# Optimization experiments

Measured on AMD Instinct MI355X. Metric: run time of the kernel, lower is better.

The kernel has to match this reference:

```python
import jax, jax.numpy as jnp
import numpy as np

ALPHA = 1.702
LIMIT = 7.0
EPS = 1e-5
TOP_K = 4


def setup_inputs() -> dict:
    key = jax.random.key(0)
    ks = jax.random.split(key, 8)
    B, S, H, I, E = 2, 512, 2048, 2048, 16
    return {
        "x": jax.random.normal(ks[0], (B, S, H), jnp.float32),
        "norm_w": jnp.ones((H,), jnp.float32),
        "gate_w": jax.random.normal(ks[1], (E, H), jnp.float32) * 0.02,
        "gate_b": jax.random.normal(ks[2], (E,), jnp.float32) * 0.02,
        "w1": jax.random.normal(ks[3], (E, 2 * I, H), jnp.float32) * 0.02,
        "b1": jax.random.normal(ks[4], (E, 2 * I), jnp.float32) * 0.02,
        "w2": jax.random.normal(ks[5], (E, H, I), jnp.float32) * 0.02,
        "b2": jax.random.normal(ks[6], (E, H), jnp.float32) * 0.02,
    }


def reference(x, norm_w, gate_w, gate_b, w1, b1, w2, b2):
    B, S, H = x.shape
    M = B * S
    E = gate_w.shape[0]
    xf = x.reshape(M, H)
    # RMSNorm
    t = xf * jax.lax.rsqrt(jnp.mean(xf * xf, axis=-1, keepdims=True) + EPS) * norm_w
    # Router: top-k over logits, then softmax over the selected k (sm_first=False)
    logits = t @ gate_w.T + gate_b  # [M, E]
    vals, idx = jax.lax.top_k(logits, TOP_K)
    gates_k = jax.nn.softmax(vals, axis=-1)  # [M, k]
    # Scatter top-k gate weights into dense [M, E] combine matrix
    G = jnp.zeros((M, E), x.dtype).at[jnp.arange(M)[:, None], idx].set(gates_k)
    # Expert MLP1 (all experts, combined sparsely below): [E, M, 2I]
    h = jnp.einsum('mh,eoh->emo', t, w1) + b1[:, None, :]
    # SwiGLU with clamp (gpt-oss): interleaved gate/linear columns
    a = jnp.minimum(h[..., ::2], LIMIT)
    b = jnp.clip(h[..., 1::2], -LIMIT, LIMIT)
    act = a * jax.nn.sigmoid(ALPHA * a) * (b + 1.0)  # [E, M, I]
    # Expert MLP2: [E, M, H]
    y = jnp.einsum('emi,edi->emd', act, w2) + b2[:, None, :]
    # Combine with gate weights (gammas scale full per-expert output incl. bias)
    delta = jnp.einsum('me,emd->md', G, y)
    return x + delta.reshape(B, S, H)
```

## Files before the change

### kernel.cpp

```cpp
#include <hip/hip_runtime.h>
#include <hip/hip_bf16.h>

constexpr int MTOK = 1024;
constexpr int HDIM = 2048;
constexpr int IDIM = 2048;
constexpr int NEXP = 16;
constexpr int TOPK = 4;
constexpr int NA   = MTOK * TOPK;

#define ALPHA_C 1.702f
#define LIMIT_C 7.0f
#define RMS_EPS 1e-5f

using short8 = __attribute__((ext_vector_type(8))) short;
using f32x4  = __attribute__((ext_vector_type(4))) float;

__device__ __forceinline__ unsigned short f2bf(float f) {
    unsigned u = __builtin_bit_cast(unsigned, f);
    u += 0x7fffu + ((u >> 16) & 1u);
    return (unsigned short)(u >> 16);
}

__device__ __forceinline__ unsigned pack2bf(float lo, float hi) {
    return (unsigned)f2bf(lo) | ((unsigned)f2bf(hi) << 16);
}

__device__ __forceinline__ short8 cvt8(const float4 a, const float4 b) {
    union { short8 s; unsigned u[4]; } r;
    r.u[0] = pack2bf(a.x, a.y);
    r.u[1] = pack2bf(a.z, a.w);
    r.u[2] = pack2bf(b.x, b.y);
    r.u[3] = pack2bf(b.z, b.w);
    return r.s;
}

__global__ __launch_bounds__(256) void k_router(
    const float* __restrict__ x, const float* __restrict__ norm_w,
    const float* __restrict__ gate_w, const float* __restrict__ gate_b,
    unsigned short* __restrict__ t_bf,
    int* __restrict__ counts, int* __restrict__ idx_of,
    int* __restrict__ slot_of, float* __restrict__ gate_mk)
{
    __shared__ float t_lds[HDIM];
    __shared__ float red[4];
    __shared__ float logits[NEXP];

    const int m   = blockIdx.x;
    const int tid = threadIdx.x;
    const float* xr = x + (size_t)m * HDIM;

    float4 v0 = ((const float4*)xr)[tid * 2];
    float4 v1 = ((const float4*)xr)[tid * 2 + 1];
    float ss = v0.x*v0.x + v0.y*v0.y + v0.z*v0.z + v0.w*v0.w
             + v1.x*v1.x + v1.y*v1.y + v1.z*v1.z + v1.w*v1.w;
    #pragma unroll
    for (int off = 32; off > 0; off >>= 1) ss += __shfl_down(ss, off);
    if ((tid & 63) == 0) red[tid >> 6] = ss;
    __syncthreads();
    float tot = red[0] + red[1] + red[2] + red[3];
    float scale = rsqrtf(tot / (float)HDIM + RMS_EPS);

    float4 n0 = ((const float4*)norm_w)[tid * 2];
    float4 n1 = ((const float4*)norm_w)[tid * 2 + 1];
    float t[8];
    t[0]=v0.x*scale*n0.x; t[1]=v0.y*scale*n0.y; t[2]=v0.z*scale*n0.z; t[3]=v0.w*scale*n0.w;
    t[4]=v1.x*scale*n1.x; t[5]=v1.y*scale*n1.y; t[6]=v1.z*scale*n1.z; t[7]=v1.w*scale*n1.w;
    short8 pk;
    #pragma unroll
    for (int j = 0; j < 8; ++j) {
        t_lds[tid * 8 + j] = t[j];
        pk[j] = (short)f2bf(t[j]);
    }
    *(short8*)(t_bf + (size_t)m * HDIM + tid * 8) = pk;
    __syncthreads();

    const int e = tid >> 4, j = tid & 15;
    const float4* gw4 = (const float4*)(gate_w + (size_t)e * HDIM);
    const float4* tl4 = (const float4*)t_lds;
    float part = 0.f;
    for (int h4 = j; h4 < HDIM / 4; h4 += 16) {
        float4 g = gw4[h4], tv = tl4[h4];
        part += g.x*tv.x + g.y*tv.y + g.z*tv.z + g.w*tv.w;
    }
    #pragma unroll
    for (int off = 8; off > 0; off >>= 1) part += __shfl_xor(part, off);
    if (j == 0) logits[e] = part + gate_b[e];
    __syncthreads();

    if (tid == 0) {
        float lv[NEXP];
        #pragma unroll
        for (int q = 0; q < NEXP; ++q) lv[q] = logits[q];
        int   sel[TOPK];
        float sv[TOPK];
        #pragma unroll
        for (int k = 0; k < TOPK; ++k) {
            float best = -1e30f; int bi = 0;
            for (int q = 0; q < NEXP; ++q)
                if (lv[q] > best) { best = lv[q]; bi = q; }
            sel[k] = bi; sv[k] = best; lv[bi] = -1e30f;
        }
        float mx = sv[0], s = 0.f, g[TOPK];
        #pragma unroll
        for (int k = 0; k < TOPK; ++k) { g[k] = __expf(sv[k] - mx); s += g[k]; }
        float inv = 1.f / s;
        #pragma unroll
        for (int k = 0; k < TOPK; ++k) {
            int a = m * TOPK + k;
            int slot = atomicAdd(&counts[sel[k]], 1);
            idx_of[a]  = sel[k];
            slot_of[a] = slot;
            gate_mk[a] = g[k] * inv;
        }
    }
}

__global__ void k_remap(const int* __restrict__ idx_of, const int* __restrict__ slot_of,
                        const int* __restrict__ counts,
                        int* __restrict__ token_of, int* __restrict__ rowidx)
{
    int a = blockIdx.x * blockDim.x + threadIdx.x;
    if (a >= NA) return;
    int e = idx_of[a];
    int off = 0;
    for (int q = 0; q < NEXP; ++q) off += (q < e) ? counts[q] : 0;
    int r = off + slot_of[a];
    token_of[r] = a >> 2;
    rowidx[a]   = r;
}

__global__ __launch_bounds__(256, 2) void k_gemm1(
    const unsigned short* __restrict__ t_bf,
    const float* __restrict__ w1, const float* __restrict__ b1,
    const int* __restrict__ counts, const int* __restrict__ token_of,
    unsigned short* __restrict__ act)
{
    __shared__ unsigned char lB[2][5120];

    const int e = blockIdx.z;
    int ne = 0, roff = 0;
    #pragma unroll
    for (int q = 0; q < NEXP; ++q) {
        int cq = counts[q];
        roff += (q < e) ? cq : 0;
        ne    = (q == e) ? cq : ne;
    }
    const int brow = blockIdx.y * 320;
    if (brow >= ne) return;
    const int i0 = blockIdx.x * 32;
    const int tid = threadIdx.x;

    const int wv = tid >> 6, ln = tid & 63;
    const int lr = ln & 15, lk = ln >> 4;
    const int br = tid >> 2, bp = tid & 3;

    const unsigned short* aptr[5];
    #pragma unroll
    for (int mf = 0; mf < 5; ++mf) {
        int rg = brow + wv * 80 + mf * 16 + lr;
        int tok = token_of[roff + (rg < ne ? rg : 0)];
        aptr[mf] = t_bf + (size_t)tok * HDIM + lk * 8;
    }
    const int o = (br < 32) ? (2 * (i0 + br)) : (2 * (i0 + br - 32) + 1);
    const float* bsrc = w1 + ((size_t)e * (2 * IDIM) + o) * HDIM + bp * 8;

    short8 aE[5], aO[5];
    float4 bS0[2], bS1[2], bS2[2], bS3[2];
    f32x4  acc[5][4] = {};

    constexpr int NT = 64;

    #pragma unroll
    for (int mf = 0; mf < 5; ++mf) aE[mf] = *(const short8*)(aptr[mf]);
    {
        float4 p0 = *(const float4*)(bsrc);
        float4 p1 = *(const float4*)(bsrc + 4);
        *(short8*)(&lB[0][br * 80 + bp * 16]) = cvt8(p0, p1);
    }
    bS1[0] = *(const float4*)(bsrc + 32);  bS1[1] = *(const float4*)(bsrc + 36);
    bS2[0] = *(const float4*)(bsrc + 64);  bS2[1] = *(const float4*)(bsrc + 68);
    asm volatile("s_waitcnt lgkmcnt(0)" ::: "memory");
    __builtin_amdgcn_s_barrier();

#define GSTEP(T_, AU, AP, SPUB, SISS)                                                    \
    {                                                                                    \
        const int t_ = (T_);                                                             \
        if (t_ + 1 < NT) {                                          \
            _Pragma("unroll")                                                            \
            for (int mf = 0; mf < 5; ++mf)                                               \
                AP[mf] = *(const short8*)(aptr[mf] + (t_ + 1) * 32);                     \
        }                                                                                \
        if (t_ + 3 < NT) {                                         \
            SISS[0] = *(const float4*)(bsrc + (t_ + 3) * 32);                            \
            SISS[1] = *(const float4*)(bsrc + (t_ + 3) * 32 + 4);                        \
        }                                                                                \
        __builtin_amdgcn_sched_barrier(0);                      \
        if (t_ + 1 < NT)                                          \
            *(short8*)(&lB[(t_ + 1) & 1][br * 80 + bp * 16]) = cvt8(SPUB[0], SPUB[1]);   \
        short8 bfr[4];                                            \
        _Pragma("unroll")                                                                \
        for (int n = 0; n < 4; ++n)                                                      \
            bfr[n] = *(const short8*)(&lB[t_ & 1][(n * 16 + lr) * 80 + lk * 16]);        \
        _Pragma("unroll")                                                                \
        for (int mf = 0; mf < 5; ++mf)                                                   \
            _Pragma("unroll")                                                            \
            for (int n = 0; n < 4; ++n)                                                  \
                acc[mf][n] = __builtin_amdgcn_mfma_f32_16x16x32_bf16(                    \
                    AU[mf], bfr[n], acc[mf][n], 0, 0, 0);                                \
        asm volatile("s_waitcnt lgkmcnt(0)" ::: "memory");                               \
        __builtin_amdgcn_s_barrier();                                                    \
    }

    for (int t4 = 0; t4 < NT / 4; ++t4) {
        const int tb = t4 * 4;
        GSTEP(tb + 0, aE, aO, bS1, bS3)
        GSTEP(tb + 1, aO, aE, bS2, bS0)
        GSTEP(tb + 2, aE, aO, bS3, bS1)
        GSTEP(tb + 3, aO, aE, bS0, bS2)
    }
#undef GSTEP

    #pragma unroll
    for (int n = 0; n < 2; ++n) {
        const int i = i0 + n * 16 + lr;
        const float ba = b1[(size_t)e * (2 * IDIM) + 2 * i];
        const float bb = b1[(size_t)e * (2 * IDIM) + 2 * i + 1];
        #pragma unroll
        for (int mf = 0; mf < 5; ++mf) {
            #pragma unroll
            for (int r = 0; r < 4; ++r) {
                const int rg = brow + wv * 80 + mf * 16 + lk * 4 + r;
                if (rg < ne) {
                    float ha = acc[mf][n][r] + ba;
                    float hb = acc[mf][n + 2][r] + bb;
                    float a = fminf(ha, LIMIT_C);
                    float b = fminf(fmaxf(hb, -LIMIT_C), LIMIT_C);
                    float s = 1.f / (1.f + __expf(-ALPHA_C * a));
                    act[(size_t)(roff + rg) * IDIM + i] = f2bf(a * s * (b + 1.f));
                }
            }
        }
    }
}

__global__ __launch_bounds__(256, 2) void k_gemm2(
    const unsigned short* __restrict__ act,
    const float* __restrict__ w2, const float* __restrict__ b2,
    const int* __restrict__ counts, const int* __restrict__ token_of,
    unsigned short* __restrict__ ybuf)
{
    __shared__ unsigned char lB[2][5120];

    const int e = blockIdx.z;
    int ne = 0, roff = 0;
    #pragma unroll
    for (int q = 0; q < NEXP; ++q) {
        int cq = counts[q];
        roff += (q < e) ? cq : 0;
        ne    = (q == e) ? cq : ne;
    }
    const int brow = blockIdx.y * 320;
    if (brow >= ne) return;
    const int d0 = blockIdx.x * 64;
    const int tid = threadIdx.x;

    const int wv = tid >> 6, ln = tid & 63;
    const int lr = ln & 15, lk = ln >> 4;
    const int br = tid >> 2, bp = tid & 3;

    const unsigned short* aptr[5];
    #pragma unroll
    for (int mf = 0; mf < 5; ++mf) {
        int rg = brow + wv * 80 + mf * 16 + lr;
        int rc = (rg < ne) ? rg : 0;
        aptr[mf] = act + (size_t)(roff + rc) * IDIM + lk * 8;
    }
    const float* bsrc = w2 + ((size_t)e * HDIM + d0 + br) * IDIM + bp * 8;

    short8 aE[5], aO[5];
    float4 bS0[2], bS1[2], bS2[2], bS3[2];
    f32x4  acc[5][4] = {};

    constexpr int NT = 64;

    #pragma unroll
    for (int mf = 0; mf < 5; ++mf) aE[mf] = *(const short8*)(aptr[mf]);
    {
        float4 p0 = *(const float4*)(bsrc);
        float4 p1 = *(const float4*)(bsrc + 4);
        *(short8*)(&lB[0][br * 80 + bp * 16]) = cvt8(p0, p1);
    }
    bS1[0] = *(const float4*)(bsrc + 32);  bS1[1] = *(const float4*)(bsrc + 36);
    bS2[0] = *(const float4*)(bsrc + 64);  bS2[1] = *(const float4*)(bsrc + 68);
    asm volatile("s_waitcnt lgkmcnt(0)" ::: "memory");
    __builtin_amdgcn_s_barrier();

#define GSTEP(T_, AU, AP, SPUB, SISS)                                                    \
    {                                                                                    \
        const int t_ = (T_);                                                             \
        if (t_ + 1 < NT) {                                                               \
            _Pragma("unroll")                                                            \
            for (int mf = 0; mf < 5; ++mf)                                               \
                AP[mf] = *(const short8*)(aptr[mf] + (t_ + 1) * 32);                     \
        }                                                                                \
        if (t_ + 3 < NT) {                                                               \
            SISS[0] = *(const float4*)(bsrc + (t_ + 3) * 32);                            \
            SISS[1] = *(const float4*)(bsrc + (t_ + 3) * 32 + 4);                        \
        }                                                                                \
        __builtin_amdgcn_sched_barrier(0);                                               \
        if (t_ + 1 < NT)                                                                 \
            *(short8*)(&lB[(t_ + 1) & 1][br * 80 + bp * 16]) = cvt8(SPUB[0], SPUB[1]);   \
        short8 bfr[4];                                                                   \
        _Pragma("unroll")                                                                \
        for (int n = 0; n < 4; ++n)                                                      \
            bfr[n] = *(const short8*)(&lB[t_ & 1][(n * 16 + lr) * 80 + lk * 16]);        \
        _Pragma("unroll")                                                                \
        for (int mf = 0; mf < 5; ++mf)                                                   \
            _Pragma("unroll")                                                            \
            for (int n = 0; n < 4; ++n)                                                  \
                acc[mf][n] = __builtin_amdgcn_mfma_f32_16x16x32_bf16(                    \
                    AU[mf], bfr[n], acc[mf][n], 0, 0, 0);                                \
        asm volatile("s_waitcnt lgkmcnt(0)" ::: "memory");                               \
        __builtin_amdgcn_s_barrier();                                                    \
    }

    for (int t4 = 0; t4 < NT / 4; ++t4) {
        const int tb = t4 * 4;
        GSTEP(tb + 0, aE, aO, bS1, bS3)
        GSTEP(tb + 1, aO, aE, bS2, bS0)
        GSTEP(tb + 2, aE, aO, bS3, bS1)
        GSTEP(tb + 3, aO, aE, bS0, bS2)
    }
#undef GSTEP

    #pragma unroll
    for (int mf = 0; mf < 5; ++mf) {
        #pragma unroll
        for (int r = 0; r < 4; ++r) {
            const int rg = brow + wv * 80 + mf * 16 + lk * 4 + r;
            if (rg >= ne) continue;
            unsigned short* yrow = ybuf + (size_t)(roff + rg) * HDIM;
            #pragma unroll
            for (int n = 0; n < 4; ++n) {
                const int d = d0 + n * 16 + lr;
                yrow[d] = f2bf(acc[mf][n][r] + b2[(size_t)e * HDIM + d]);
            }
        }
    }
}

__global__ __launch_bounds__(256) void k_comb(
    const float* __restrict__ x, const unsigned short* __restrict__ ybuf,
    const int* __restrict__ rowidx, const float* __restrict__ gate_mk,
    float* __restrict__ out)
{
    __shared__ int   rws[TOPK];
    __shared__ float gws[TOPK];
    const int m = blockIdx.x;
    const int tid = threadIdx.x;
    if (tid < TOPK) {
        rws[tid] = rowidx[m * TOPK + tid];
        gws[tid] = gate_mk[m * TOPK + tid];
    }
    __syncthreads();
    const int d = tid * 8;
    float4 o0 = ((const float4*)(x + (size_t)m * HDIM + d))[0];
    float4 o1 = ((const float4*)(x + (size_t)m * HDIM + d))[1];
    #pragma unroll
    for (int k = 0; k < TOPK; ++k) {
        const float g = gws[k];
        short8 y = *(const short8*)(ybuf + (size_t)rws[k] * HDIM + d);
        float yv[8];
        #pragma unroll
        for (int j = 0; j < 8; ++j) {
            unsigned u = ((unsigned)(unsigned short)y[j]) << 16;
            yv[j] = __builtin_bit_cast(float, u);
        }
        o0.x += g * yv[0]; o0.y += g * yv[1]; o0.z += g * yv[2]; o0.w += g * yv[3];
        o1.x += g * yv[4]; o1.y += g * yv[5]; o1.z += g * yv[6]; o1.w += g * yv[7];
    }
    ((float4*)(out + (size_t)m * HDIM + d))[0] = o0;
    ((float4*)(out + (size_t)m * HDIM + d))[1] = o1;
}

extern "C" void kernel_launch(void* const* d_in, const int* in_sizes, int n_in,
                              void* d_out, int out_size, void* d_ws, size_t ws_size,
                              hipStream_t stream) {
    const float* x      = (const float*)d_in[0];
    const float* norm_w = (const float*)d_in[1];
    const float* gate_w = (const float*)d_in[2];
    const float* gate_b = (const float*)d_in[3];
    const float* w1     = (const float*)d_in[4];
    const float* b1     = (const float*)d_in[5];
    const float* w2     = (const float*)d_in[6];
    const float* b2     = (const float*)d_in[7];
    float* out = (float*)d_out;

    char* ws = (char*)d_ws;
    size_t off = 0;
    unsigned short* t_bf = (unsigned short*)(ws + off); off += (size_t)MTOK * HDIM * 2;
    unsigned short* actb = (unsigned short*)(ws + off); off += (size_t)NA * IDIM * 2;
    unsigned short* ybuf = (unsigned short*)(ws + off); off += (size_t)NA * HDIM * 2;
    int*   counts   = (int*)(ws + off);   off += 256;
    int*   idx_of   = (int*)(ws + off);   off += (size_t)NA * 4;
    int*   slot_of  = (int*)(ws + off);   off += (size_t)NA * 4;
    float* gate_mk  = (float*)(ws + off); off += (size_t)NA * 4;
    int*   token_of = (int*)(ws + off);   off += (size_t)NA * 4;
    int*   rowidx   = (int*)(ws + off);   off += (size_t)NA * 4;

    (void)hipMemsetAsync(counts, 0, 256, stream);
    k_router<<<MTOK, 256, 0, stream>>>(x, norm_w, gate_w, gate_b, t_bf,
                                       counts, idx_of, slot_of, gate_mk);
    k_remap<<<NA / 256, 256, 0, stream>>>(idx_of, slot_of, counts,
                                          token_of, rowidx);
    k_gemm1<<<dim3(IDIM / 32, (MTOK + 319) / 320, NEXP), 256, 0, stream>>>(
        t_bf, w1, b1, counts, token_of, actb);
    k_gemm2<<<dim3(HDIM / 64, (MTOK + 319) / 320, NEXP), 256, 0, stream>>>(
        actb, w2, b2, counts, token_of, ybuf);
    k_comb<<<MTOK, 256, 0, stream>>>(x, ybuf, rowidx, gate_mk, out);
}
```

Before: 410.9 us.

## Stage fp32 weight tiles via direct global-to-LDS loads with 4-deep XOR-swizzled buffers

Both expert GEMM kernels now copy the fp32 weight tiles straight into LDS with global_load_lds, using a 4-stage ring buffer and an XOR swizzle, instead of loading into registers, converting to bf16 and storing to LDS. The fp32-to-bf16 conversion moves to after the LDS read. The goal is to cut register pressure and VALU work in the load path and to keep more loads in flight, with explicit vmcnt waits. In exchange, LDS use doubles (fp32 staging, 4 buffers), LDS read traffic per step doubles, and each wave repeats the conversion work, which may hurt occupancy.

```diff
diff --git a/kernel.cpp b/kernel.cpp
--- a/kernel.cpp
+++ b/kernel.cpp
@@ -33,6 +33,17 @@
     r.u[3] = pack2bf(b.z, b.w);
     return r.s;
 }
+
+__device__ __forceinline__ void gload16(const void* g, void* l) {
+    __builtin_amdgcn_global_load_lds(
+        (const __attribute__((address_space(1))) void*)g,
+        (__attribute__((address_space(3))) void*)l, 16, 0, 0);
+}
+
+#define WAITV(n)  asm volatile("s_waitcnt vmcnt(" #n ")" ::: "memory")
+#define WAITL0    asm volatile("s_waitcnt lgkmcnt(0)" ::: "memory")
+#define BARRIER   asm volatile("s_barrier" ::: "memory")
+#define SCHEDB    __builtin_amdgcn_sched_barrier(0)
 
 __global__ __launch_bounds__(256) void k_router(
     const float* __restrict__ x, const float* __restrict__ norm_w,
@@ -135,7 +146,7 @@
     const int* __restrict__ counts, const int* __restrict__ token_of,
     unsigned short* __restrict__ act)
 {
-    __shared__ unsigned char lB[2][5120];
+    __shared__ float lB[4][2048];
 
     const int e = blockIdx.z;
     int ne = 0, roff = 0;
@@ -152,7 +163,6 @@
 
     const int wv = tid >> 6, ln = tid & 63;
     const int lr = ln & 15, lk = ln >> 4;
-    const int br = tid >> 2, bp = tid & 3;
 
     const unsigned short* aptr[5];
     #pragma unroll
@@ -161,64 +171,84 @@
         int tok = token_of[roff + (rg < ne ? rg : 0)];
         aptr[mf] = t_bf + (size_t)tok * HDIM + lk * 8;
     }
-    const int o = (br < 32) ? (2 * (i0 + br)) : (2 * (i0 + br - 32) + 1);
-    const float* bsrc = w1 + ((size_t)e * (2 * IDIM) + o) * HDIM + bp * 8;
+
+    const int cj0 = (wv * 2 + 0) * 8 + (ln >> 3);
+    const int cj1 = (wv * 2 + 1) * 8 + (ln >> 3);
+    const int c2  = ln & 7;
+    const int o0 = (cj0 < 32) ? (2 * (i0 + cj0)) : (2 * (i0 + cj0 - 32) + 1);
+    const int o1 = (cj1 < 32) ? (2 * (i0 + cj1)) : (2 * (i0 + cj1 - 32) + 1);
+    const float* bs0 = w1 + ((size_t)e * (2 * IDIM) + o0) * HDIM + (c2 ^ (cj0 & 7)) * 4;
+    const float* bs1 = w1 + ((size_t)e * (2 * IDIM) + o1) * HDIM + (c2 ^ (cj1 & 7)) * 4;
+    float* lw0 = &lB[0][(wv * 2 + 0) * 256];
+    float* lw1 = &lB[0][(wv * 2 + 1) * 256];
 
     short8 aE[5], aO[5];
-    float4 bS0[2], bS1[2], bS2[2], bS3[2];
     f32x4  acc[5][4] = {};
-
     constexpr int NT = 64;
 
-    #pragma unroll
-    for (int mf = 0; mf < 5; ++mf) aE[mf] = *(const short8*)(aptr[mf]);
-    {
-        float4 p0 = *(const float4*)(bsrc);
-        float4 p1 = *(const float4*)(bsrc + 4);
-        *(short8*)(&lB[0][br * 80 + bp * 16]) = cvt8(p0, p1);
-    }
-    bS1[0] = *(const float4*)(bsrc + 32);  bS1[1] = *(const float4*)(bsrc + 36);
-    bS2[0] = *(const float4*)(bsrc + 64);  bS2[1] = *(const float4*)(bsrc + 68);
-    asm volatile("s_waitcnt lgkmcnt(0)" ::: "memory");
-    __builtin_amdgcn_s_barrier();
-
-#define GSTEP(T_, AU, AP, SPUB, SISS)                                                    \
+#define STAGE1(T_) { gload16(bs0 + (T_) * 32, lw0 + ((T_) & 3) * 2048); \
+                     gload16(bs1 + (T_) * 32, lw1 + ((T_) & 3) * 2048); }
+
+#define COMPUTE1(T_, AU)                                                                 \
     {                                                                                    \
-        const int t_ = (T_);                                                             \
-        if (t_ + 1 < NT) {                                          \
-            _Pragma("unroll")                                                            \
-            for (int mf = 0; mf < 5; ++mf)                                               \
-                AP[mf] = *(const short8*)(aptr[mf] + (t_ + 1) * 32);                     \
+        short8 bfr[4];                                                                   \
+        _Pragma("unroll")                                                                \
+        for (int n = 0; n < 4; ++n) {                                                    \
+            const int c_ = n * 16 + lr;                                                  \
+            const float* cb = &lB[(T_) & 3][0] + c_ * 32;                                \
+            float4 u0 = *(const float4*)(cb + (((2 * lk)     ^ (c_ & 7)) * 4));          \
+            float4 u1 = *(const float4*)(cb + (((2 * lk + 1) ^ (c_ & 7)) * 4));          \
+            bfr[n] = cvt8(u0, u1);                                                       \
         }                                                                                \
-        if (t_ + 3 < NT) {                                         \
-            SISS[0] = *(const float4*)(bsrc + (t_ + 3) * 32);                            \
-            SISS[1] = *(const float4*)(bsrc + (t_ + 3) * 32 + 4);                        \
-        }                                                                                \
-        __builtin_amdgcn_sched_barrier(0);                      \
-        if (t_ + 1 < NT)                                          \
-            *(short8*)(&lB[(t_ + 1) & 1][br * 80 + bp * 16]) = cvt8(SPUB[0], SPUB[1]);   \
-        short8 bfr[4];                                            \
-        _Pragma("unroll")                                                                \
-        for (int n = 0; n < 4; ++n)                                                      \
-            bfr[n] = *(const short8*)(&lB[t_ & 1][(n * 16 + lr) * 80 + lk * 16]);        \
         _Pragma("unroll")                                                                \
         for (int mf = 0; mf < 5; ++mf)                                                   \
             _Pragma("unroll")                                                            \
             for (int n = 0; n < 4; ++n)                                                  \
                 acc[mf][n] = __builtin_amdgcn_mfma_f32_16x16x32_bf16(                    \
                     AU[mf], bfr[n], acc[mf][n], 0, 0, 0);                                \
-        asm volatile("s_waitcnt lgkmcnt(0)" ::: "memory");                               \
-        __builtin_amdgcn_s_barrier();                                                    \
-    }
-
-    for (int t4 = 0; t4 < NT / 4; ++t4) {
-        const int tb = t4 * 4;
-        GSTEP(tb + 0, aE, aO, bS1, bS3)
-        GSTEP(tb + 1, aO, aE, bS2, bS0)
-        GSTEP(tb + 2, aE, aO, bS3, bS1)
-        GSTEP(tb + 3, aO, aE, bS0, bS2)
-    }
-#undef GSTEP
+    }
+
+#define LOADA1(T_, AP)                                                                   \
+    {                                                                                    \
+        _Pragma("unroll")                                                                \
+        for (int mf = 0; mf < 5; ++mf)                                                   \
+            AP[mf] = *(const short8*)(aptr[mf] + (T_) * 32);                             \
+    }
+
+    STAGE1(0) STAGE1(1)
+    SCHEDB;
+    LOADA1(0, aE)
+    SCHEDB;
+    STAGE1(2)
+    SCHEDB;
+    WAITV(9);
+    BARRIER;
+
+    for (int t2 = 0; t2 < 30; ++t2) {
+        const int t = t2 * 2;
+        LOADA1(t + 1, aO) SCHEDB;
+        STAGE1(t + 3)     SCHEDB;
+        WAITV(9); SCHEDB;
+        COMPUTE1(t, aE)
+        WAITL0; BARRIER;
+        LOADA1(t + 2, aE) SCHEDB;
+        STAGE1(t + 4)     SCHEDB;
+        WAITV(9); SCHEDB;
+        COMPUTE1(t + 1, aO)
+        WAITL0; BARRIER;
+    }
+    LOADA1(61, aO) SCHEDB; STAGE1(63) SCHEDB; WAITV(9); SCHEDB;
+    COMPUTE1(60, aE) WAITL0; BARRIER;
+    LOADA1(62, aE) SCHEDB; WAITV(7); SCHEDB;
+    COMPUTE1(61, aO) WAITL0; BARRIER;
+    LOADA1(63, aO) SCHEDB; WAITV(5); SCHEDB;
+    COMPUTE1(62, aE) WAITL0; BARRIER;
+    WAITV(0); SCHEDB;
+    COMPUTE1(63, aO)
+
+#undef STAGE1
+#undef COMPUTE1
+#undef LOADA1
 
     #pragma unroll
     for (int n = 0; n < 2; ++n) {
@@ -249,7 +279,7 @@
     const int* __restrict__ counts, const int* __restrict__ token_of,
     unsigned short* __restrict__ ybuf)
 {
-    __shared__ unsigned char lB[2][5120];
+    __shared__ float lB[4][2048];
 
     const int e = blockIdx.z;
     int ne = 0, roff = 0;
@@ -266,7 +296,6 @@
 
     const int wv = tid >> 6, ln = tid & 63;
     const int lr = ln & 15, lk = ln >> 4;
-    const int br = tid >> 2, bp = tid & 3;
 
     const unsigned short* aptr[5];
     #pragma unroll
@@ -275,63 +304,83 @@
         int rc = (rg < ne) ? rg : 0;
         aptr[mf] = act + (size_t)(roff + rc) * IDIM + lk * 8;
     }
-    const float* bsrc = w2 + ((size_t)e * HDIM + d0 + br) * IDIM + bp * 8;
+
+    const int cj0 = (wv * 2 + 0) * 8 + (ln >> 3);
+    const int cj1 = (wv * 2 + 1) * 8 + (ln >> 3);
+    const int c2  = ln & 7;
+    const float* bs0 = w2 + ((size_t)e * HDIM + d0 + cj0) * IDIM + (c2 ^ (cj0 & 7)) * 4;
+    const float* bs1 = w2 + ((size_t)e * HDIM + d0 + cj1) * IDIM + (c2 ^ (cj1 & 7)) * 4;
+    float* lw0 = &lB[0][(wv * 2 + 0) * 256];
+    float* lw1 = &lB[0][(wv * 2 + 1) * 256];
 
     short8 aE[5], aO[5];
-    float4 bS0[2], bS1[2], bS2[2], bS3[2];
     f32x4  acc[5][4] = {};
-
     constexpr int NT = 64;
-
-    #pragma unroll
-    for (int mf = 0; mf < 5; ++mf) aE[mf] = *(const short8*)(aptr[mf]);
-    {
-        float4 p0 = *(const float4*)(bsrc);
-        float4 p1 = *(const float4*)(bsrc + 4);
-        *(short8*)(&lB[0][br * 80 + bp * 16]) = cvt8(p0, p1);
-    }
-    bS1[0] = *(const float4*)(bsrc + 32);  bS1[1] = *(const float4*)(bsrc + 36);
-    bS2[0] = *(const float4*)(bsrc + 64);  bS2[1] = *(const float4*)(bsrc + 68);
-    asm volatile("s_waitcnt lgkmcnt(0)" ::: "memory");
-    __builtin_amdgcn_s_barrier();
-
-#define GSTEP(T_, AU, AP, SPUB, SISS)                                                    \
+    (void)NT;
+
+#define STAGE2(T_) { gload16(bs0 + (T_) * 32, lw0 + ((T_) & 3) * 2048); \
+                     gload16(bs1 + (T_) * 32, lw1 + ((T_) & 3) * 2048); }
+
+#define COMPUTE2(T_, AU)                                                                 \
     {                                                                                    \
-        const int t_ = (T_);                                                             \
-        if (t_ + 1 < NT) {                                                               \
-            _Pragma("unroll")                                                            \
-            for (int mf = 0; mf < 5; ++mf)                                               \
-                AP[mf] = *(const short8*)(aptr[mf] + (t_ + 1) * 32);                     \
+        short8 bfr[4];                                                                   \
+        _Pragma("unroll")                                                                \
+        for (int n = 0; n < 4; ++n) {                                                    \
+            const int c_ = n * 16 + lr;                                                  \
+            const float* cb = &lB[(T_) & 3][0] + c_ * 32;                                \
+            float4 u0 = *(const float4*)(cb + (((2 * lk)     ^ (c_ & 7)) * 4));          \
+            float4 u1 = *(const float4*)(cb + (((2 * lk + 1) ^ (c_ & 7)) * 4));          \
+            bfr[n] = cvt8(u0, u1);                                                       \
         }                                                                                \
-        if (t_ + 3 < NT) {                                                               \
-            SISS[0] = *(const float4*)(bsrc + (t_ + 3) * 32);                            \
-            SISS[1] = *(const float4*)(bsrc + (t_ + 3) * 32 + 4);                        \
-        }                                                                                \
-        __builtin_amdgcn_sched_barrier(0);                                               \
-        if (t_ + 1 < NT)                                                                 \
-            *(short8*)(&lB[(t_ + 1) & 1][br * 80 + bp * 16]) = cvt8(SPUB[0], SPUB[1]);   \
-        short8 bfr[4];                                                                   \
-        _Pragma("unroll")                                                                \
-        for (int n = 0; n < 4; ++n)                                                      \
-            bfr[n] = *(const short8*)(&lB[t_ & 1][(n * 16 + lr) * 80 + lk * 16]);        \
         _Pragma("unroll")                                                                \
         for (int mf = 0; mf < 5; ++mf)                                                   \
             _Pragma("unroll")                                                            \
             for (int n = 0; n < 4; ++n)                                                  \
                 acc[mf][n] = __builtin_amdgcn_mfma_f32_16x16x32_bf16(                    \
                     AU[mf], bfr[n], acc[mf][n], 0, 0, 0);                                \
-        asm volatile("s_waitcnt lgkmcnt(0)" ::: "memory");                               \
-        __builtin_amdgcn_s_barrier();                                                    \
-    }
-
-    for (int t4 = 0; t4 < NT / 4; ++t4) {
-        const int tb = t4 * 4;
-        GSTEP(tb + 0, aE, aO, bS1, bS3)
-        GSTEP(tb + 1, aO, aE, bS2, bS0)
-        GSTEP(tb + 2, aE, aO, bS3, bS1)
-        GSTEP(tb + 3, aO, aE, bS0, bS2)
-    }
-#undef GSTEP
+    }
+
+#define LOADA2(T_, AP)                                                                   \
+    {                                                                                    \
+        _Pragma("unroll")                                                                \
+        for (int mf = 0; mf < 5; ++mf)                                                   \
+            AP[mf] = *(const short8*)(aptr[mf] + (T_) * 32);                             \
+    }
+
+    STAGE2(0) STAGE2(1)
+    SCHEDB;
+    LOADA2(0, aE)
+    SCHEDB;
+    STAGE2(2)
+    SCHEDB;
+    WAITV(9);
+    BARRIER;
+
+    for (int t2 = 0; t2 < 30; ++t2) {
+        const int t = t2 * 2;
+        LOADA2(t + 1, aO) SCHEDB;
+        STAGE2(t + 3)     SCHEDB;
+        WAITV(9); SCHEDB;
+        COMPUTE2(t, aE)
+        WAITL0; BARRIER;
+        LOADA2(t + 2, aE) SCHEDB;
+        STAGE2(t + 4)     SCHEDB;
+        WAITV(9); SCHEDB;
+        COMPUTE2(t + 1, aO)
+        WAITL0; BARRIER;
+    }
+    LOADA2(61, aO) SCHEDB; STAGE2(63) SCHEDB; WAITV(9); SCHEDB;
+    COMPUTE2(60, aE) WAITL0; BARRIER;
+    LOADA2(62, aE) SCHEDB; WAITV(7); SCHEDB;
+    COMPUTE2(61, aO) WAITL0; BARRIER;
+    LOADA2(63, aO) SCHEDB; WAITV(5); SCHEDB;
+    COMPUTE2(62, aE) WAITL0; BARRIER;
+    WAITV(0); SCHEDB;
+    COMPUTE2(63, aO)
+
+#undef STAGE2
+#undef COMPUTE2
+#undef LOADA2
 
     #pragma unroll
     for (int mf = 0; mf < 5; ++mf) {
```

After: 416.8 us. About the same (+1.4%).

## Stage 256-wide K chunks of fp32 weights per barrier in both expert GEMMs

Applied to the files above, without the earlier changes.

Both expert GEMM kernels now stage a 256-element K slab of weights per thread (16 float4 loads of contiguous memory) into a larger double-buffered LDS tile, and run 8 MFMA sub-steps between barriers instead of one. This cuts the barrier count from 64 to 8 per tile and gives each thread longer contiguous global reads. In exchange it raises LDS use to about 68KB per block and adds 64 staging registers per thread, which may reduce occupancy given launch_bounds(256,2).

```diff
diff --git a/kernel.cpp b/kernel.cpp
--- a/kernel.cpp
+++ b/kernel.cpp
@@ -33,6 +33,9 @@
     r.u[3] = pack2bf(b.z, b.w);
     return r.s;
 }
+
+#define WAITL0    asm volatile("s_waitcnt lgkmcnt(0)" ::: "memory")
+#define BARRIER   asm volatile("s_barrier" ::: "memory")
 
 __global__ __launch_bounds__(256) void k_router(
     const float* __restrict__ x, const float* __restrict__ norm_w,
@@ -135,7 +138,7 @@
     const int* __restrict__ counts, const int* __restrict__ token_of,
     unsigned short* __restrict__ act)
 {
-    __shared__ unsigned char lB[2][5120];
+    __shared__ unsigned char lB[2][64 * 544];
 
     const int e = blockIdx.z;
     int ne = 0, roff = 0;
@@ -152,7 +155,7 @@
 
     const int wv = tid >> 6, ln = tid & 63;
     const int lr = ln & 15, lk = ln >> 4;
-    const int br = tid >> 2, bp = tid & 3;
+    const int col = tid >> 2, q4 = tid & 3;
 
     const unsigned short* aptr[5];
     #pragma unroll
@@ -161,64 +164,55 @@
         int tok = token_of[roff + (rg < ne ? rg : 0)];
         aptr[mf] = t_bf + (size_t)tok * HDIM + lk * 8;
     }
-    const int o = (br < 32) ? (2 * (i0 + br)) : (2 * (i0 + br - 32) + 1);
-    const float* bsrc = w1 + ((size_t)e * (2 * IDIM) + o) * HDIM + bp * 8;
-
+    const int o = (col < 32) ? (2 * (i0 + col)) : (2 * (i0 + col - 32) + 1);
+    const float4* bcol = (const float4*)(w1 + ((size_t)e * (2 * IDIM) + o) * HDIM) + q4 * 16;
+
+    float4 sv[16];
     short8 aE[5], aO[5];
-    float4 bS0[2], bS1[2], bS2[2], bS3[2];
     f32x4  acc[5][4] = {};
 
-    constexpr int NT = 64;
-
-    #pragma unroll
-    for (int mf = 0; mf < 5; ++mf) aE[mf] = *(const short8*)(aptr[mf]);
-    {
-        float4 p0 = *(const float4*)(bsrc);
-        float4 p1 = *(const float4*)(bsrc + 4);
-        *(short8*)(&lB[0][br * 80 + bp * 16]) = cvt8(p0, p1);
-    }
-    bS1[0] = *(const float4*)(bsrc + 32);  bS1[1] = *(const float4*)(bsrc + 36);
-    bS2[0] = *(const float4*)(bsrc + 64);  bS2[1] = *(const float4*)(bsrc + 68);
-    asm volatile("s_waitcnt lgkmcnt(0)" ::: "memory");
-    __builtin_amdgcn_s_barrier();
-
-#define GSTEP(T_, AU, AP, SPUB, SISS)                                                    \
-    {                                                                                    \
-        const int t_ = (T_);                                                             \
-        if (t_ + 1 < NT) {                                          \
-            _Pragma("unroll")                                                            \
-            for (int mf = 0; mf < 5; ++mf)                                               \
-                AP[mf] = *(const short8*)(aptr[mf] + (t_ + 1) * 32);                     \
-        }                                                                                \
-        if (t_ + 3 < NT) {                                         \
-            SISS[0] = *(const float4*)(bsrc + (t_ + 3) * 32);                            \
-            SISS[1] = *(const float4*)(bsrc + (t_ + 3) * 32 + 4);                        \
-        }                                                                                \
-        __builtin_amdgcn_sched_barrier(0);                      \
-        if (t_ + 1 < NT)                                          \
-            *(short8*)(&lB[(t_ + 1) & 1][br * 80 + bp * 16]) = cvt8(SPUB[0], SPUB[1]);   \
-        short8 bfr[4];                                            \
-        _Pragma("unroll")                                                                \
-        for (int n = 0; n < 4; ++n)                                                      \
-            bfr[n] = *(const short8*)(&lB[t_ & 1][(n * 16 + lr) * 80 + lk * 16]);        \
-        _Pragma("unroll")                                                                \
-        for (int mf = 0; mf < 5; ++mf)                                                   \
-            _Pragma("unroll")                                                            \
-            for (int n = 0; n < 4; ++n)                                                  \
-                acc[mf][n] = __builtin_amdgcn_mfma_f32_16x16x32_bf16(                    \
-                    AU[mf], bfr[n], acc[mf][n], 0, 0, 0);                                \
-        asm volatile("s_waitcnt lgkmcnt(0)" ::: "memory");                               \
-        __builtin_amdgcn_s_barrier();                                                    \
-    }
-
-    for (int t4 = 0; t4 < NT / 4; ++t4) {
-        const int tb = t4 * 4;
-        GSTEP(tb + 0, aE, aO, bS1, bS3)
-        GSTEP(tb + 1, aO, aE, bS2, bS0)
-        GSTEP(tb + 2, aE, aO, bS3, bS1)
-        GSTEP(tb + 3, aO, aE, bS0, bS2)
-    }
-#undef GSTEP
+#define STAGE(T_)                                                                        \
+    { _Pragma("unroll") for (int j = 0; j < 16; ++j) sv[j] = bcol[(T_) * 64 + j]; }
+
+#define PUBLISH(T_)                                                                      \
+    { unsigned char* Lw = lB[(T_) & 1] + col * 544 + q4 * 128;                           \
+      _Pragma("unroll") for (int s = 0; s < 8; ++s)                                      \
+          *(short8*)(Lw + s * 16) = cvt8(sv[2 * s], sv[2 * s + 1]); }
+
+#define LOADA(G_, AP)                                                                    \
+    { _Pragma("unroll") for (int mf = 0; mf < 5; ++mf)                                   \
+          AP[mf] = *(const short8*)(aptr[mf] + (G_) * 32); }
+
+#define SUB(T_, KS, AU, AP)                                                              \
+    { if ((T_) * 8 + (KS) + 1 < 64) LOADA((T_) * 8 + (KS) + 1, AP)                       \
+      short8 bfr[4];                                                                     \
+      unsigned char* Lr = lB[(T_) & 1];                                                  \
+      _Pragma("unroll") for (int n = 0; n < 4; ++n)                                      \
+          bfr[n] = *(const short8*)(Lr + (n * 16 + lr) * 544 + ((KS) * 4 + lk) * 16);    \
+      _Pragma("unroll") for (int mf = 0; mf < 5; ++mf)                                   \
+          _Pragma("unroll") for (int n = 0; n < 4; ++n)                                  \
+              acc[mf][n] = __builtin_amdgcn_mfma_f32_16x16x32_bf16(                      \
+                  AU[mf], bfr[n], acc[mf][n], 0, 0, 0); }
+
+    STAGE(0)
+    PUBLISH(0)
+    LOADA(0, aE)
+    WAITL0; BARRIER;
+
+    for (int t = 0; t < 8; ++t) {
+        if (t + 1 < 8) STAGE(t + 1)
+        SUB(t, 0, aE, aO) SUB(t, 1, aO, aE)
+        SUB(t, 2, aE, aO) SUB(t, 3, aO, aE)
+        SUB(t, 4, aE, aO) SUB(t, 5, aO, aE)
+        SUB(t, 6, aE, aO) SUB(t, 7, aO, aE)
+        if (t + 1 < 8) PUBLISH(t + 1)
+        WAITL0; BARRIER;
+    }
+
+#undef STAGE
+#undef PUBLISH
+#undef LOADA
+#undef SUB
 
     #pragma unroll
     for (int n = 0; n < 2; ++n) {
@@ -249,7 +243,7 @@
     const int* __restrict__ counts, const int* __restrict__ token_of,
     unsigned short* __restrict__ ybuf)
 {
-    __shared__ unsigned char lB[2][5120];
+    __shared__ unsigned char lB[2][64 * 544];
 
     const int e = blockIdx.z;
     int ne = 0, roff = 0;
@@ -266,7 +260,7 @@
 
     const int wv = tid >> 6, ln = tid & 63;
     const int lr = ln & 15, lk = ln >> 4;
-    const int br = tid >> 2, bp = tid & 3;
+    const int col = tid >> 2, q4 = tid & 3;
 
     const unsigned short* aptr[5];
     #pragma unroll
@@ -275,63 +269,54 @@
         int rc = (rg < ne) ? rg : 0;
         aptr[mf] = act + (size_t)(roff + rc) * IDIM + lk * 8;
     }
-    const float* bsrc = w2 + ((size_t)e * HDIM + d0 + br) * IDIM + bp * 8;
-
+    const float4* bcol = (const float4*)(w2 + ((size_t)e * HDIM + d0 + col) * IDIM) + q4 * 16;
+
+    float4 sv[16];
     short8 aE[5], aO[5];
-    float4 bS0[2], bS1[2], bS2[2], bS3[2];
     f32x4  acc[5][4] = {};
 
-    constexpr int NT = 64;
-
-    #pragma unroll
-    for (int mf = 0; mf < 5; ++mf) aE[mf] = *(const short8*)(aptr[mf]);
-    {
-        float4 p0 = *(const float4*)(bsrc);
-        float4 p1 = *(const float4*)(bsrc + 4);
-        *(short8*)(&lB[0][br * 80 + bp * 16]) = cvt8(p0, p1);
-    }
-    bS1[0] = *(const float4*)(bsrc + 32);  bS1[1] = *(const float4*)(bsrc + 36);
-    bS2[0] = *(const float4*)(bsrc + 64);  bS2[1] = *(const float4*)(bsrc + 68);
-    asm volatile("s_waitcnt lgkmcnt(0)" ::: "memory");
-    __builtin_amdgcn_s_barrier();
-
-#define GSTEP(T_, AU, AP, SPUB, SISS)                                                    \
-    {                                                                                    \
-        const int t_ = (T_);                                                             \
-        if (t_ + 1 < NT) {                                                               \
-            _Pragma("unroll")                                                            \
-            for (int mf = 0; mf < 5; ++mf)                                               \
-                AP[mf] = *(const short8*)(aptr[mf] + (t_ + 1) * 32);                     \
-        }                                                                                \
-        if (t_ + 3 < NT) {                                                               \
-            SISS[0] = *(const float4*)(bsrc + (t_ + 3) * 32);                            \
-            SISS[1] = *(const float4*)(bsrc + (t_ + 3) * 32 + 4);                        \
-        }                                                                                \
-        __builtin_amdgcn_sched_barrier(0);                                               \
-        if (t_ + 1 < NT)                                                                 \
-            *(short8*)(&lB[(t_ + 1) & 1][br * 80 + bp * 16]) = cvt8(SPUB[0], SPUB[1]);   \
-        short8 bfr[4];                                                                   \
-        _Pragma("unroll")                                                                \
-        for (int n = 0; n < 4; ++n)                                                      \
-            bfr[n] = *(const short8*)(&lB[t_ & 1][(n * 16 + lr) * 80 + lk * 16]);        \
-        _Pragma("unroll")                                                                \
-        for (int mf = 0; mf < 5; ++mf)                                                   \
-            _Pragma("unroll")                                                            \
-            for (int n = 0; n < 4; ++n)                                                  \
-                acc[mf][n] = __builtin_amdgcn_mfma_f32_16x16x32_bf16(                    \
-                    AU[mf], bfr[n], acc[mf][n], 0, 0, 0);                                \
-        asm volatile("s_waitcnt lgkmcnt(0)" ::: "memory");                               \
-        __builtin_amdgcn_s_barrier();                                                    \
-    }
-
-    for (int t4 = 0; t4 < NT / 4; ++t4) {
-        const int tb = t4 * 4;
-        GSTEP(tb + 0, aE, aO, bS1, bS3)
-        GSTEP(tb + 1, aO, aE, bS2, bS0)
-        GSTEP(tb + 2, aE, aO, bS3, bS1)
-        GSTEP(tb + 3, aO, aE, bS0, bS2)
-    }
-#undef GSTEP
+#define STAGE(T_)                                                                        \
+    { _Pragma("unroll") for (int j = 0; j < 16; ++j) sv[j] = bcol[(T_) * 64 + j]; }
+
+#define PUBLISH(T_)                                                                      \
+    { unsigned char* Lw = lB[(T_) & 1] + col * 544 + q4 * 128;                           \
+      _Pragma("unroll") for (int s = 0; s < 8; ++s)                                      \
+          *(short8*)(Lw + s * 16) = cvt8(sv[2 * s], sv[2 * s + 1]); }
+
+#define LOADA(G_, AP)                                                                    \
+    { _Pragma("unroll") for (int mf = 0; mf < 5; ++mf)                                   \
+          AP[mf] = *(const short8*)(aptr[mf] + (G_) * 32); }
+
+#define SUB(T_, KS, AU, AP)                                                              \
+    { if ((T_) * 8 + (KS) + 1 < 64) LOADA((T_) * 8 + (KS) + 1, AP)                       \
+      short8 bfr[4];                                                                     \
+      unsigned char* Lr = lB[(T_) & 1];                                                  \
+      _Pragma("unroll") for (int n = 0; n < 4; ++n)                                      \
+          bfr[n] = *(const short8*)(Lr + (n * 16 + lr) * 544 + ((KS) * 4 + lk) * 16);    \
+      _Pragma("unroll") for (int mf = 0; mf < 5; ++mf)                                   \
+          _Pragma("unroll") for (int n = 0; n < 4; ++n)                                  \
+              acc[mf][n] = __builtin_amdgcn_mfma_f32_16x16x32_bf16(                      \
+                  AU[mf], bfr[n], acc[mf][n], 0, 0, 0); }
+
+    STAGE(0)
+    PUBLISH(0)
+    LOADA(0, aE)
+    WAITL0; BARRIER;
+
+    for (int t = 0; t < 8; ++t) {
+        if (t + 1 < 8) STAGE(t + 1)
+        SUB(t, 0, aE, aO) SUB(t, 1, aO, aE)
+        SUB(t, 2, aE, aO) SUB(t, 3, aO, aE)
+        SUB(t, 4, aE, aO) SUB(t, 5, aO, aE)
+        SUB(t, 6, aE, aO) SUB(t, 7, aO, aE)
+        if (t + 1 < 8) PUBLISH(t + 1)
+        WAITL0; BARRIER;
+    }
+
+#undef STAGE
+#undef PUBLISH
+#undef LOADA
+#undef SUB
 
     #pragma unroll
     for (int mf = 0; mf < 5; ++mf) {
```

Result: slower. 429.1 us (+4.4%).

## Pre-gather A into K-major layout and give each wave private B tiles

Applied to the files above, without the earlier changes.

Two new kernels are added. One gathers routed token rows into a K-chunk-major buffer before GEMM1, and one transposes the activations into the same layout before GEMM2, so the A-fragment loads in both GEMMs become coalesced. Each wave now loads, converts and stages its own B tile in a private LDS slice, which removes the block-wide barriers but makes every wave re-read the same weights (4x redundant global B traffic). The occupancy hint of 2 blocks per CU is dropped. The price is extra launches and extra write/read passes over multi-MB intermediate buffers.

```diff
diff --git a/kernel.cpp b/kernel.cpp
--- a/kernel.cpp
+++ b/kernel.cpp
@@ -13,25 +13,13 @@
 #define RMS_EPS 1e-5f
 
 using short8 = __attribute__((ext_vector_type(8))) short;
+using sh4    = __attribute__((ext_vector_type(4))) short;
 using f32x4  = __attribute__((ext_vector_type(4))) float;
 
 __device__ __forceinline__ unsigned short f2bf(float f) {
     unsigned u = __builtin_bit_cast(unsigned, f);
     u += 0x7fffu + ((u >> 16) & 1u);
     return (unsigned short)(u >> 16);
-}
-
-__device__ __forceinline__ unsigned pack2bf(float lo, float hi) {
-    return (unsigned)f2bf(lo) | ((unsigned)f2bf(hi) << 16);
-}
-
-__device__ __forceinline__ short8 cvt8(const float4 a, const float4 b) {
-    union { short8 s; unsigned u[4]; } r;
-    r.u[0] = pack2bf(a.x, a.y);
-    r.u[1] = pack2bf(a.z, a.w);
-    r.u[2] = pack2bf(b.x, b.y);
-    r.u[3] = pack2bf(b.z, b.w);
-    return r.s;
 }
 
 __global__ __launch_bounds__(256) void k_router(
@@ -129,13 +117,45 @@
     rowidx[a]   = r;
 }
 
-__global__ __launch_bounds__(256, 2) void k_gemm1(
-    const unsigned short* __restrict__ t_bf,
+__global__ __launch_bounds__(256) void k_gatherA(
+    const unsigned short* __restrict__ t_bf, const int* __restrict__ token_of,
+    unsigned short* __restrict__ tA)
+{
+    const int tid = threadIdx.x;
+    const int r   = tid & 63, kci = tid >> 6;
+    const int R0  = blockIdx.x * 64;
+    const int tok = token_of[R0 + r];
+    const unsigned short* src = t_bf + (size_t)tok * HDIM;
+    #pragma unroll 4
+    for (int j = 0; j < 64; ++j) {
+        const int kc = kci + 4 * j;
+        short8 v = *(const short8*)(src + kc * 8);
+        *(short8*)(tA + ((size_t)kc * NA + R0 + r) * 8) = v;
+    }
+}
+
+__global__ __launch_bounds__(256) void k_transT(
+    const unsigned short* __restrict__ act, unsigned short* __restrict__ actT)
+{
+    const int tid = threadIdx.x;
+    const int r   = tid & 63, kci = tid >> 6;
+    const int R0  = blockIdx.x * 64;
+    const unsigned short* src = act + (size_t)(R0 + r) * IDIM;
+    #pragma unroll 4
+    for (int j = 0; j < 64; ++j) {
+        const int kc = kci + 4 * j;
+        short8 v = *(const short8*)(src + kc * 8);
+        *(short8*)(actT + ((size_t)kc * NA + R0 + r) * 8) = v;
+    }
+}
+
+__global__ __launch_bounds__(256) void k_gemm1(
+    const unsigned short* __restrict__ tA,
     const float* __restrict__ w1, const float* __restrict__ b1,
-    const int* __restrict__ counts, const int* __restrict__ token_of,
+    const int* __restrict__ counts,
     unsigned short* __restrict__ act)
 {
-    __shared__ unsigned char lB[2][5120];
+    __shared__ unsigned char lB[4][2][5120];
 
     const int e = blockIdx.z;
     int ne = 0, roff = 0;
@@ -152,73 +172,65 @@
 
     const int wv = tid >> 6, ln = tid & 63;
     const int lr = ln & 15, lk = ln >> 4;
-    const int br = tid >> 2, bp = tid & 3;
-
-    const unsigned short* aptr[5];
+    const int cb = ln >> 3, q8 = ln & 7;
+
+    const unsigned short* aptrK[5];
     #pragma unroll
     for (int mf = 0; mf < 5; ++mf) {
         int rg = brow + wv * 80 + mf * 16 + lr;
-        int tok = token_of[roff + (rg < ne ? rg : 0)];
-        aptr[mf] = t_bf + (size_t)tok * HDIM + lk * 8;
-    }
-    const int o = (br < 32) ? (2 * (i0 + br)) : (2 * (i0 + br - 32) + 1);
-    const float* bsrc = w1 + ((size_t)e * (2 * IDIM) + o) * HDIM + bp * 8;
+        int r  = roff + (rg < ne ? rg : 0);
+        aptrK[mf] = tA + ((size_t)lk * NA + r) * 8;
+    }
+    const float* bptr[8];
+    #pragma unroll
+    for (int j = 0; j < 8; ++j) {
+        int c = cb + 8 * j;
+        int o = (c < 32) ? (2 * (i0 + c)) : (2 * (i0 + c - 32) + 1);
+        bptr[j] = w1 + ((size_t)e * (2 * IDIM) + o) * HDIM + q8 * 4;
+    }
+    unsigned char* Lw = &lB[wv][0][0];
 
     short8 aE[5], aO[5];
-    float4 bS0[2], bS1[2], bS2[2], bS3[2];
+    f32x4  bE[8], bO[8];
     f32x4  acc[5][4] = {};
-
     constexpr int NT = 64;
 
-    #pragma unroll
-    for (int mf = 0; mf < 5; ++mf) aE[mf] = *(const short8*)(aptr[mf]);
-    {
-        float4 p0 = *(const float4*)(bsrc);
-        float4 p1 = *(const float4*)(bsrc + 4);
-        *(short8*)(&lB[0][br * 80 + bp * 16]) = cvt8(p0, p1);
-    }
-    bS1[0] = *(const float4*)(bsrc + 32);  bS1[1] = *(const float4*)(bsrc + 36);
-    bS2[0] = *(const float4*)(bsrc + 64);  bS2[1] = *(const float4*)(bsrc + 68);
-    asm volatile("s_waitcnt lgkmcnt(0)" ::: "memory");
-    __builtin_amdgcn_s_barrier();
-
-#define GSTEP(T_, AU, AP, SPUB, SISS)                                                    \
+#define STEP(T_, AC, AN, BC, BN)                                                         \
     {                                                                                    \
         const int t_ = (T_);                                                             \
-        if (t_ + 1 < NT) {                                          \
-            _Pragma("unroll")                                                            \
-            for (int mf = 0; mf < 5; ++mf)                                               \
-                AP[mf] = *(const short8*)(aptr[mf] + (t_ + 1) * 32);                     \
+        if (t_ + 1 < NT) {                                                               \
+            _Pragma("unroll") for (int mf = 0; mf < 5; ++mf)                             \
+                AN[mf] = *(const short8*)(aptrK[mf] + (size_t)(t_ + 1) * (4 * NA * 8));  \
+            _Pragma("unroll") for (int j = 0; j < 8; ++j)                                \
+                BN[j] = *(const f32x4*)(bptr[j] + (t_ + 1) * 32);                        \
         }                                                                                \
-        if (t_ + 3 < NT) {                                         \
-            SISS[0] = *(const float4*)(bsrc + (t_ + 3) * 32);                            \
-            SISS[1] = *(const float4*)(bsrc + (t_ + 3) * 32 + 4);                        \
+        __builtin_amdgcn_sched_barrier(0);                                               \
+        _Pragma("unroll") for (int j = 0; j < 8; ++j) {                                  \
+            sh4 w; w[0] = (short)f2bf(BC[j][0]); w[1] = (short)f2bf(BC[j][1]);           \
+                   w[2] = (short)f2bf(BC[j][2]); w[3] = (short)f2bf(BC[j][3]);           \
+            *(sh4*)(Lw + (t_ & 1) * 5120 + (cb + 8 * j) * 80 + q8 * 8) = w;              \
         }                                                                                \
-        __builtin_amdgcn_sched_barrier(0);                      \
-        if (t_ + 1 < NT)                                          \
-            *(short8*)(&lB[(t_ + 1) & 1][br * 80 + bp * 16]) = cvt8(SPUB[0], SPUB[1]);   \
-        short8 bfr[4];                                            \
-        _Pragma("unroll")                                                                \
-        for (int n = 0; n < 4; ++n)                                                      \
-            bfr[n] = *(const short8*)(&lB[t_ & 1][(n * 16 + lr) * 80 + lk * 16]);        \
-        _Pragma("unroll")                                                                \
-        for (int mf = 0; mf < 5; ++mf)                                                   \
-            _Pragma("unroll")                                                            \
-            for (int n = 0; n < 4; ++n)                                                  \
+        asm volatile("s_waitcnt lgkmcnt(0)" ::: "memory");                               \
+        __builtin_amdgcn_sched_barrier(0);                                               \
+        short8 bfr[4];                                                                   \
+        _Pragma("unroll") for (int n = 0; n < 4; ++n)                                    \
+            bfr[n] = *(const short8*)(Lw + (t_ & 1) * 5120 + (n * 16 + lr) * 80 + lk * 16);\
+        _Pragma("unroll") for (int mf = 0; mf < 5; ++mf)                                 \
+            _Pragma("unroll") for (int n = 0; n < 4; ++n)                                \
                 acc[mf][n] = __builtin_amdgcn_mfma_f32_16x16x32_bf16(                    \
-                    AU[mf], bfr[n], acc[mf][n], 0, 0, 0);                                \
-        asm volatile("s_waitcnt lgkmcnt(0)" ::: "memory");                               \
-        __builtin_amdgcn_s_barrier();                                                    \
-    }
-
-    for (int t4 = 0; t4 < NT / 4; ++t4) {
-        const int tb = t4 * 4;
-        GSTEP(tb + 0, aE, aO, bS1, bS3)
-        GSTEP(tb + 1, aO, aE, bS2, bS0)
-        GSTEP(tb + 2, aE, aO, bS3, bS1)
-        GSTEP(tb + 3, aO, aE, bS0, bS2)
-    }
-#undef GSTEP
+                    AC[mf], bfr[n], acc[mf][n], 0, 0, 0);                                \
+    }
+
+    #pragma unroll
+    for (int mf = 0; mf < 5; ++mf) aE[mf] = *(const short8*)(aptrK[mf]);
+    #pragma unroll
+    for (int j = 0; j < 8; ++j) bE[j] = *(const f32x4*)(bptr[j]);
+
+    for (int t2 = 0; t2 < NT / 2; ++t2) {
+        STEP(2 * t2,     aE, aO, bE, bO)
+        STEP(2 * t2 + 1, aO, aE, bO, bE)
+    }
+#undef STEP
 
     #pragma unroll
     for (int n = 0; n < 2; ++n) {
@@ -243,13 +255,13 @@
     }
 }
 
-__global__ __launch_bounds__(256, 2) void k_gemm2(
-    const unsigned short* __restrict__ act,
+__global__ __launch_bounds__(256) void k_gemm2(
+    const unsigned short* __restrict__ actT,
     const float* __restrict__ w2, const float* __restrict__ b2,
-    const int* __restrict__ counts, const int* __restrict__ token_of,
+    const int* __restrict__ counts,
     unsigned short* __restrict__ ybuf)
 {
-    __shared__ unsigned char lB[2][5120];
+    __shared__ unsigned char lB[4][2][5120];
 
     const int e = blockIdx.z;
     int ne = 0, roff = 0;
@@ -266,72 +278,64 @@
 
     const int wv = tid >> 6, ln = tid & 63;
     const int lr = ln & 15, lk = ln >> 4;
-    const int br = tid >> 2, bp = tid & 3;
-
-    const unsigned short* aptr[5];
+    const int cb = ln >> 3, q8 = ln & 7;
+
+    const unsigned short* aptrK[5];
     #pragma unroll
     for (int mf = 0; mf < 5; ++mf) {
         int rg = brow + wv * 80 + mf * 16 + lr;
-        int rc = (rg < ne) ? rg : 0;
-        aptr[mf] = act + (size_t)(roff + rc) * IDIM + lk * 8;
-    }
-    const float* bsrc = w2 + ((size_t)e * HDIM + d0 + br) * IDIM + bp * 8;
+        int r  = roff + (rg < ne ? rg : 0);
+        aptrK[mf] = actT + ((size_t)lk * NA + r) * 8;
+    }
+    const float* bptr[8];
+    #pragma unroll
+    for (int j = 0; j < 8; ++j) {
+        int c = cb + 8 * j;
+        bptr[j] = w2 + ((size_t)e * HDIM + d0 + c) * IDIM + q8 * 4;
+    }
+    unsigned char* Lw = &lB[wv][0][0];
 
     short8 aE[5], aO[5];
-    float4 bS0[2], bS1[2], bS2[2], bS3[2];
+    f32x4  bE[8], bO[8];
     f32x4  acc[5][4] = {};
-
     constexpr int NT = 64;
 
-    #pragma unroll
-    for (int mf = 0; mf < 5; ++mf) aE[mf] = *(const short8*)(aptr[mf]);
-    {
-        float4 p0 = *(const float4*)(bsrc);
-        float4 p1 = *(const float4*)(bsrc + 4);
-        *(short8*)(&lB[0][br * 80 + bp * 16]) = cvt8(p0, p1);
-    }
-    bS1[0] = *(const float4*)(bsrc + 32);  bS1[1] = *(const float4*)(bsrc + 36);
-    bS2[0] = *(const float4*)(bsrc + 64);  bS2[1] = *(const float4*)(bsrc + 68);
-    asm volatile("s_waitcnt lgkmcnt(0)" ::: "memory");
-    __builtin_amdgcn_s_barrier();
-
-#define GSTEP(T_, AU, AP, SPUB, SISS)                                                    \
+#define STEP(T_, AC, AN, BC, BN)                                                         \
     {                                                                                    \
         const int t_ = (T_);                                                             \
         if (t_ + 1 < NT) {                                                               \
-            _Pragma("unroll")                                                            \
-            for (int mf = 0; mf < 5; ++mf)                                               \
-                AP[mf] = *(const short8*)(aptr[mf] + (t_ + 1) * 32);                     \
-        }                                                                                \
-        if (t_ + 3 < NT) {                                                               \
-            SISS[0] = *(const float4*)(bsrc + (t_ + 3) * 32);                            \
-            SISS[1] = *(const float4*)(bsrc + (t_ + 3) * 32 + 4);                        \
+            _Pragma("unroll") for (int mf = 0; mf < 5; ++mf)                             \
+                AN[mf] = *(const short8*)(aptrK[mf] + (size_t)(t_ + 1) * (4 * NA * 8));  \
+            _Pragma("unroll") for (int j = 0; j < 8; ++j)                                \
+                BN[j] = *(const f32x4*)(bptr[j] + (t_ + 1) * 32);                        \
         }                                                                                \
         __builtin_amdgcn_sched_barrier(0);                                               \
-        if (t_ + 1 < NT)                                                                 \
-            *(short8*)(&lB[(t_ + 1) & 1][br * 80 + bp * 16]) = cvt8(SPUB[0], SPUB[1]);   \
+        _Pragma("unroll") for (int j = 0; j < 8; ++j) {                                  \
+            sh4 w; w[0] = (short)f2bf(BC[j][0]); w[1] = (short)f2bf(BC[j][1]);           \
+                   w[2] = (short)f2bf(BC[j][2]); w[3] = (short)f2bf(BC[j][3]);           \
+            *(sh4*)(Lw + (t_ & 1) * 5120 + (cb + 8 * j) * 80 + q8 * 8) = w;              \
+        }                                                                                \
+        asm volatile("s_waitcnt lgkmcnt(0)" ::: "memory");                               \
+        __builtin_amdgcn_sched_barrier(0);                                               \
         short8 bfr[4];                                                                   \
-        _Pragma("unroll")                                                                \
-        for (int n = 0; n < 4; ++n)                                                      \
-            bfr[n] = *(const short8*)(&lB[t_ & 1][(n * 16 + lr) * 80 + lk * 16]);        \
-        _Pragma("unroll")                                                                \
-        for (int mf = 0; mf < 5; ++mf)                                                   \
-            _Pragma("unroll")                                                            \
-            for (int n = 0; n < 4; ++n)                                                  \
+        _Pragma("unroll") for (int n = 0; n < 4; ++n)                                    \
+            bfr[n] = *(const short8*)(Lw + (t_ & 1) * 5120 + (n * 16 + lr) * 80 + lk * 16);\
+        _Pragma("unroll") for (int mf = 0; mf < 5; ++mf)                                 \
+            _Pragma("unroll") for (int n = 0; n < 4; ++n)                                \
                 acc[mf][n] = __builtin_amdgcn_mfma_f32_16x16x32_bf16(                    \
-                    AU[mf], bfr[n], acc[mf][n], 0, 0, 0);                                \
-        asm volatile("s_waitcnt lgkmcnt(0)" ::: "memory");                               \
-        __builtin_amdgcn_s_barrier();                                                    \
-    }
-
-    for (int t4 = 0; t4 < NT / 4; ++t4) {
-        const int tb = t4 * 4;
-        GSTEP(tb + 0, aE, aO, bS1, bS3)
-        GSTEP(tb + 1, aO, aE, bS2, bS0)
-        GSTEP(tb + 2, aE, aO, bS3, bS1)
-        GSTEP(tb + 3, aO, aE, bS0, bS2)
-    }
-#undef GSTEP
+                    AC[mf], bfr[n], acc[mf][n], 0, 0, 0);                                \
+    }
+
+    #pragma unroll
+    for (int mf = 0; mf < 5; ++mf) aE[mf] = *(const short8*)(aptrK[mf]);
+    #pragma unroll
+    for (int j = 0; j < 8; ++j) bE[j] = *(const f32x4*)(bptr[j]);
+
+    for (int t2 = 0; t2 < NT / 2; ++t2) {
+        STEP(2 * t2,     aE, aO, bE, bO)
+        STEP(2 * t2 + 1, aO, aE, bO, bE)
+    }
+#undef STEP
 
     #pragma unroll
     for (int mf = 0; mf < 5; ++mf) {
@@ -399,7 +403,9 @@
     char* ws = (char*)d_ws;
     size_t off = 0;
     unsigned short* t_bf = (unsigned short*)(ws + off); off += (size_t)MTOK * HDIM * 2;
+    unsigned short* tA   = (unsigned short*)(ws + off); off += (size_t)NA * HDIM * 2;
     unsigned short* actb = (unsigned short*)(ws + off); off += (size_t)NA * IDIM * 2;
+    unsigned short* actT = (unsigned short*)(ws + off); off += (size_t)NA * IDIM * 2;
     unsigned short* ybuf = (unsigned short*)(ws + off); off += (size_t)NA * HDIM * 2;
     int*   counts   = (int*)(ws + off);   off += 256;
     int*   idx_of   = (int*)(ws + off);   off += (size_t)NA * 4;
@@ -413,9 +419,11 @@
                                        counts, idx_of, slot_of, gate_mk);
     k_remap<<<NA / 256, 256, 0, stream>>>(idx_of, slot_of, counts,
                                           token_of, rowidx);
+    k_gatherA<<<NA / 64, 256, 0, stream>>>(t_bf, token_of, tA);
     k_gemm1<<<dim3(IDIM / 32, (MTOK + 319) / 320, NEXP), 256, 0, stream>>>(
-        t_bf, w1, b1, counts, token_of, actb);
+        tA, w1, b1, counts, actb);
+    k_transT<<<NA / 64, 256, 0, stream>>>(actb, actT);
     k_gemm2<<<dim3(HDIM / 64, (MTOK + 319) / 320, NEXP), 256, 0, stream>>>(
-        actb, w2, b2, counts, token_of, ybuf);
+        actT, w2, b2, counts, ybuf);
     k_comb<<<MTOK, 256, 0, stream>>>(x, ybuf, rowidx, gate_mk, out);
 }
```

After: 434.7 us. 1.06x slower.
